# Kernel tuning notes

Measured on AMD Instinct MI355X. Metric: run time of the kernel, lower is better.

The kernel has to match this reference:

```python
import jax, jax.numpy as jnp
import numpy as np

N = 50000
IN_CH = 128
HID = 256
HEADS = 8
HEAD_DIM = HID // HEADS
NUM_CLASSES = 2
E = 800000
NEG_SLOPE = 0.2  # PyG GATConv default leaky_relu slope


def gat_conv(x, edge_index, W, att_src, att_dst, bias):
    """PyG-style GATConv (concat=True, add_self_loops=True, eval mode).
    x: [N, HID]; edge_index: [2, E] (row 0 = source j, row 1 = target i).
    W: [HID, HEADS*HEAD_DIM]; att_src/att_dst: [HEADS, HEAD_DIM]; bias: [HEADS*HEAD_DIM].
    """
    loop = jnp.arange(N)
    src = jnp.concatenate([edge_index[0], loop])  # self-loops appended
    dst = jnp.concatenate([edge_index[1], loop])
    h = (x @ W).reshape(N, HEADS, HEAD_DIM)          # [N, H, D]
    a_src = jnp.einsum('nhd,hd->nh', h, att_src)     # [N, H]
    a_dst = jnp.einsum('nhd,hd->nh', h, att_dst)
    e = jax.nn.leaky_relu(a_src[src] + a_dst[dst], NEG_SLOPE)  # [E+N, H]
    # segment softmax over incoming edges of each target node
    m = jax.ops.segment_max(e, dst, num_segments=N)
    p = jnp.exp(e - m[dst])
    s = jax.ops.segment_sum(p, dst, num_segments=N)
    alpha = p / (s[dst] + 1e-16)                     # [E+N, H]
    msg = h[src] * alpha[:, :, None]                 # [E+N, H, D]
    out = jax.ops.segment_sum(msg, dst, num_segments=N)  # [N, H, D]
    return out.reshape(N, HEADS * HEAD_DIM) + bias


def setup_inputs() -> dict:
    key = jax.random.key(0)
    ks = jax.random.split(key, 24)
    g = lambda k, shape, fan_in: jax.random.normal(k, shape, dtype=jnp.float32) / np.sqrt(fan_in)
    inp = {}
    inp['x'] = jax.random.normal(ks[0], (N, IN_CH), dtype=jnp.float32)
    inp['tut_edge_index'] = jax.random.randint(ks[1], (2, E), 0, N)
    inp['tdt_edge_index'] = jax.random.randint(ks[2], (2, E), 0, N)
    inp['proj_W'] = g(ks[3], (IN_CH, HID), IN_CH)
    inp['proj_b'] = jnp.zeros((HID,), jnp.float32)
    # 2 GAT layers per meta-path, stacked on leading axis
    inp['tut_W'] = g(ks[4], (2, HID, HID), HID)
    inp['tut_asrc'] = g(ks[5], (2, HEADS, HEAD_DIM), HEAD_DIM)
    inp['tut_adst'] = g(ks[6], (2, HEADS, HEAD_DIM), HEAD_DIM)
    inp['tut_bias'] = jnp.zeros((2, HID), jnp.float32)
    inp['tdt_W'] = g(ks[7], (2, HID, HID), HID)
    inp['tdt_asrc'] = g(ks[8], (2, HEADS, HEAD_DIM), HEAD_DIM)
    inp['tdt_adst'] = g(ks[9], (2, HEADS, HEAD_DIM), HEAD_DIM)
    inp['tdt_bias'] = jnp.zeros((2, HID), jnp.float32)
    inp['sem_att'] = jnp.full((2,), 0.5, jnp.float32)
    inp['cls_W1'] = g(ks[10], (HID, HID // 2), HID)
    inp['cls_b1'] = jnp.zeros((HID // 2,), jnp.float32)
    inp['cls_W2'] = g(ks[11], (HID // 2, NUM_CLASSES), HID // 2)
    inp['cls_b2'] = jnp.zeros((NUM_CLASSES,), jnp.float32)
    return inp


def reference(x, tut_edge_index, tdt_edge_index, proj_W, proj_b,
              tut_W, tut_asrc, tut_adst, tut_bias,
              tdt_W, tdt_asrc, tdt_adst, tdt_bias,
              sem_att, cls_W1, cls_b1, cls_W2, cls_b2):
    h = x @ proj_W + proj_b
    # TUT branch: 2 GATConv layers (eval mode -> dropout is identity)
    h_tut = h
    for l in range(2):
        h_tut = gat_conv(h_tut, tut_edge_index, tut_W[l], tut_asrc[l], tut_adst[l], tut_bias[l])
        h_tut = jax.nn.elu(h_tut)
    # TDT branch
    h_tdt = h
    for l in range(2):
        h_tdt = gat_conv(h_tdt, tdt_edge_index, tdt_W[l], tdt_asrc[l], tdt_adst[l], tdt_bias[l])
        h_tdt = jax.nn.elu(h_tdt)
    w = jax.nn.softmax(sem_att)
    z = w[0] * h_tut + w[1] * h_tdt
    hc = jax.nn.relu(z @ cls_W1 + cls_b1)
    logits = hc @ cls_W2 + cls_b2  # [N, NUM_CLASSES]
    return logits
```

## Files before the change

### kernel.cpp

```cpp
#include <hip/hip_runtime.h>
#include <hip/hip_fp16.h>
#include <cstddef>
#include <cstdint>


#define HID        256
#define HEADS      8
#define NEG_SLOPE  0.2f

#define BSH     7
#define BNODES  128
#define MAXNB   512
#define CH      2048

typedef __attribute__((ext_vector_type(8))) short short8v;
typedef __attribute__((ext_vector_type(4))) float float4v;

static __device__ __forceinline__ unsigned short f32_to_bf16(float v) {
    union { float f; unsigned u; } c; c.f = v;
    unsigned r = c.u + 0x7FFFu + ((c.u >> 16) & 1u);
    return (unsigned short)(r >> 16);
}
static __device__ __forceinline__ float bf16_to_f32(unsigned short b) {
    union { unsigned u; float f; } c; c.u = ((unsigned)b) << 16;
    return c.f;
}
static __device__ __forceinline__ void split_bf16(float v, unsigned short& hi, unsigned short& lo) {
    hi = f32_to_bf16(v);
    lo = f32_to_bf16(v - bf16_to_f32(hi));
}
static __device__ __forceinline__ void gload_lds16(const void* g, void* l) {
    __builtin_amdgcn_global_load_lds((const __attribute__((address_space(1))) void*)g,
                                     (__attribute__((address_space(3))) void*)l, 16, 0, 0);
}

template<int MODE>
__global__ __launch_bounds__(256) void mfma_gemm_kernel(
    const unsigned short* __restrict__ Ahi, const unsigned short* __restrict__ Alo,
    const unsigned short* __restrict__ Bthi, const unsigned short* __restrict__ Btlo,
    const float* __restrict__ bias,
    unsigned short* __restrict__ Chi, unsigned short* __restrict__ Clo,
    __half* __restrict__ Cf16a, __half* __restrict__ Cf16b, float* __restrict__ Cf32,
    int M, int N, int K)
{
    __shared__ __align__(16) short lds[4 * 4096];

    const int tid  = threadIdx.x;
    const int lane = tid & 63;
    const int w    = tid >> 6;
    const int wr   = w >> 1;
    const int wc   = w & 1;
    const int m0   = blockIdx.y * 128;
    const int n0   = blockIdx.x * 128;

    const unsigned short* sbase = (w == 0) ? Ahi : (w == 1) ? Alo : (w == 2) ? Bthi : Btlo;
    const int rowbase = (w < 2) ? m0 : n0;
    const int rowlim  = ((w < 2) ? M : N) - 1;

    float4v acc[4][4];
    #pragma unroll
    for (int i = 0; i < 4; ++i)
        #pragma unroll
        for (int j = 0; j < 4; ++j)
            acc[i][j] = (float4v){0.f, 0.f, 0.f, 0.f};

    const int kcl = lane >> 4;
    const int rl  = lane & 15;

    for (int k0 = 0; k0 < K; k0 += 32) {
        #pragma unroll
        for (int rh = 0; rh < 2; ++rh) {
            int row = rowbase + rh * 64 + lane;
            row = row > rowlim ? rowlim : row;
            const unsigned short* src = sbase + (size_t)row * K + k0;
            #pragma unroll
            for (int kc = 0; kc < 4; ++kc) {
                short* dst = &lds[w * 4096 + kc * 1024 + rh * 512];
                gload_lds16(src + kc * 8, dst);
            }
        }
        __syncthreads();

        short8v ahi[4], alo[4], bhi[4], blo[4];
        #pragma unroll
        for (int i = 0; i < 4; ++i) {
            int am = wr * 64 + i * 16 + rl;
            int bn = wc * 64 + i * 16 + rl;
            ahi[i] = *(const short8v*)&lds[0 * 4096 + kcl * 1024 + am * 8];
            alo[i] = *(const short8v*)&lds[1 * 4096 + kcl * 1024 + am * 8];
            bhi[i] = *(const short8v*)&lds[2 * 4096 + kcl * 1024 + bn * 8];
            blo[i] = *(const short8v*)&lds[3 * 4096 + kcl * 1024 + bn * 8];
        }
        #pragma unroll
        for (int i = 0; i < 4; ++i)
            #pragma unroll
            for (int j = 0; j < 4; ++j) {
                acc[i][j] = __builtin_amdgcn_mfma_f32_16x16x32_bf16(ahi[i], bhi[j], acc[i][j], 0, 0, 0);
                acc[i][j] = __builtin_amdgcn_mfma_f32_16x16x32_bf16(ahi[i], blo[j], acc[i][j], 0, 0, 0);
                acc[i][j] = __builtin_amdgcn_mfma_f32_16x16x32_bf16(alo[i], bhi[j], acc[i][j], 0, 0, 0);
            }
        __syncthreads();
    }

    const int cr = (lane >> 4) * 4;
    #pragma unroll
    for (int i = 0; i < 4; ++i) {
        #pragma unroll
        for (int r = 0; r < 4; ++r) {
            int row = m0 + wr * 64 + i * 16 + cr + r;
            if (row >= M) continue;
            #pragma unroll
            for (int j = 0; j < 4; ++j) {
                int col = n0 + wc * 64 + j * 16 + rl;
                float v = acc[i][j][r];
                if (bias) v += bias[col];
                if (MODE == 0) {
                    unsigned short h, l;
                    split_bf16(v, h, l);
                    Chi[(size_t)row * N + col] = h;
                    Clo[(size_t)row * N + col] = l;
                } else if (MODE == 1) {
                    if (col < 256) Cf16a[(size_t)row * 256 + col] = __float2half(v);
                    else           Cf16b[(size_t)row * 256 + (col - 256)] = __float2half(v);
                } else {
                    Cf32[(size_t)row * N + col] = fmaxf(v, 0.f);
                }
            }
        }
    }
}

__global__ void prep_kernel(
    const float* __restrict__ proj_W, const float* __restrict__ tut_W,
    const float* __restrict__ tdt_W, const float* __restrict__ cls_W1,
    unsigned short* __restrict__ pWthi, unsigned short* __restrict__ pWtlo,
    unsigned short* __restrict__ w1hi,  unsigned short* __restrict__ w1lo,
    unsigned short* __restrict__ t2Whi, unsigned short* __restrict__ t2Wlo,
    unsigned short* __restrict__ d2Whi, unsigned short* __restrict__ d2Wlo,
    unsigned short* __restrict__ cWthi, unsigned short* __restrict__ cWtlo,
    const float* __restrict__ x,
    unsigned short* __restrict__ xhi, unsigned short* __restrict__ xlo, int count4x)
{
    const int tid = blockIdx.x * blockDim.x + threadIdx.x;
    const int stride = gridDim.x * blockDim.x;
    for (int idx = tid; idx < 327680; idx += stride) {
        unsigned short h, l;
        if (idx < 32768) {
            int k = idx >> 8, n = idx & 255;
            split_bf16(proj_W[idx], h, l);
            pWthi[n * 128 + k] = h; pWtlo[n * 128 + k] = l;
        } else if (idx < 163840) {
            int r = idx - 32768;
            int ly = r >> 16, rr = r & 65535;
            int k = rr >> 8, n = rr & 255;
            split_bf16(tut_W[r], h, l);
            if (ly == 0) { w1hi[n * 256 + k] = h;  w1lo[n * 256 + k] = l; }
            else         { t2Whi[n * 256 + k] = h; t2Wlo[n * 256 + k] = l; }
        } else if (idx < 294912) {
            int r = idx - 163840;
            int ly = r >> 16, rr = r & 65535;
            int k = rr >> 8, n = rr & 255;
            split_bf16(tdt_W[r], h, l);
            if (ly == 0) { w1hi[(256 + n) * 256 + k] = h; w1lo[(256 + n) * 256 + k] = l; }
            else         { d2Whi[n * 256 + k] = h;        d2Wlo[n * 256 + k] = l; }
        } else {
            int r = idx - 294912;
            int k = r >> 7, n = r & 127;
            split_bf16(cls_W1[r], h, l);
            cWthi[n * 256 + k] = h; cWtlo[n * 256 + k] = l;
        }
    }
    for (int i = tid; i < count4x; i += stride) {
        float4 v = reinterpret_cast<const float4*>(x)[i];
        ushort4 hh, ll;
        split_bf16(v.x, hh.x, ll.x);
        split_bf16(v.y, hh.y, ll.y);
        split_bf16(v.z, hh.z, ll.z);
        split_bf16(v.w, hh.w, ll.w);
        reinterpret_cast<ushort4*>(xhi)[i] = hh;
        reinterpret_cast<ushort4*>(xlo)[i] = ll;
    }
}

__global__ __launch_bounds__(256) void att_kernel(
    const __half* __restrict__ hW,
    const float* __restrict__ att_src, const float* __restrict__ att_dst,
    float* __restrict__ a_src, float* __restrict__ a_dst, int n_nodes)
{
    const int wave = threadIdx.x >> 6;
    const int lane = threadIdx.x & 63;
    const int n = blockIdx.x * 4 + wave;
    if (n >= n_nodes) return;

    const __half2* hp = reinterpret_cast<const __half2*>(&hW[(size_t)n * HID + lane * 4]);
    __half2 h01 = hp[0], h23 = hp[1];
    float hx = __low2float(h01), hy = __high2float(h01);
    float hz = __low2float(h23), hw = __high2float(h23);
    float4 s4 = *reinterpret_cast<const float4*>(&att_src[lane * 4]);
    float4 d4 = *reinterpret_cast<const float4*>(&att_dst[lane * 4]);
    float ps = hx * s4.x + hy * s4.y + hz * s4.z + hw * s4.w;
    float pd = hx * d4.x + hy * d4.y + hz * d4.z + hw * d4.w;
    #pragma unroll
    for (int off = 1; off < 8; off <<= 1) {
        ps += __shfl_xor(ps, off);
        pd += __shfl_xor(pd, off);
    }
    if ((lane & 7) == 0) {
        a_src[n * HEADS + (lane >> 3)] = ps;
        a_dst[n * HEADS + (lane >> 3)] = pd;
    }
}

template<int OMODE>
__global__ __launch_bounds__(256) void gat_kernel(
    const __half* __restrict__ hW,
    const float* __restrict__ a_src, const float* __restrict__ a_dst,
    const int* __restrict__ row_ptr, const int* __restrict__ adj,
    const float* __restrict__ bias,
    const unsigned short* __restrict__ prevHi, const unsigned short* __restrict__ prevLo,
    const float* __restrict__ sem,
    unsigned short* __restrict__ outhi, unsigned short* __restrict__ outlo,
    int n_nodes)
{
    const int wave = threadIdx.x >> 6;
    const int lane = threadIdx.x & 63;
    const int n = blockIdx.x * 4 + wave;
    if (n >= n_nodes) return;

    const int beg = row_ptr[n];
    const int end = row_ptr[n + 1];
    const int h1 = lane & 7;
    const float adst1 = a_dst[n * HEADS + h1];

    float m = -INFINITY, s = 0.f;
    for (int j = beg + (lane >> 3); j < end; j += 8) {
        float e = a_src[adj[j] * HEADS + h1] + adst1;
        e = (e > 0.f) ? e : NEG_SLOPE * e;
        float mn = fmaxf(m, e);
        float t = (m > -INFINITY) ? s * __expf(m - mn) : 0.f;
        s = t + __expf(e - mn);
        m = mn;
    }
    #pragma unroll
    for (int off = 8; off < 64; off <<= 1) {
        float mo = __shfl_xor(m, off);
        float so = __shfl_xor(s, off);
        float mn = fmaxf(m, mo);
        float t1 = (m  > -INFINITY) ? s  * __expf(m  - mn) : 0.f;
        float t2 = (mo > -INFINITY) ? so * __expf(mo - mn) : 0.f;
        s = t1 + t2;
        m = mn;
    }

    const int h2 = lane >> 3;
    const float mh  = __shfl(m, h2);
    const float sh  = __shfl(s, h2);
    const float inv = 1.f / (sh + 1e-16f);
    const float adst2 = a_dst[n * HEADS + h2];
    const int lane4 = lane * 4;

    float4 acc = make_float4(0.f, 0.f, 0.f, 0.f);
    int j = beg;
    for (; j + 4 <= end; j += 4) {
        int s0 = adj[j + 0], s1 = adj[j + 1], s2 = adj[j + 2], s3 = adj[j + 3];
        float e0 = a_src[s0 * HEADS + h2] + adst2;
        float e1 = a_src[s1 * HEADS + h2] + adst2;
        float e2 = a_src[s2 * HEADS + h2] + adst2;
        float e3 = a_src[s3 * HEADS + h2] + adst2;
        e0 = (e0 > 0.f) ? e0 : NEG_SLOPE * e0;
        e1 = (e1 > 0.f) ? e1 : NEG_SLOPE * e1;
        e2 = (e2 > 0.f) ? e2 : NEG_SLOPE * e2;
        e3 = (e3 > 0.f) ? e3 : NEG_SLOPE * e3;
        float al0 = __expf(e0 - mh) * inv;
        float al1 = __expf(e1 - mh) * inv;
        float al2 = __expf(e2 - mh) * inv;
        float al3 = __expf(e3 - mh) * inv;
        const __half2* p0 = reinterpret_cast<const __half2*>(&hW[(size_t)s0 * HID + lane4]);
        const __half2* p1 = reinterpret_cast<const __half2*>(&hW[(size_t)s1 * HID + lane4]);
        const __half2* p2 = reinterpret_cast<const __half2*>(&hW[(size_t)s2 * HID + lane4]);
        const __half2* p3 = reinterpret_cast<const __half2*>(&hW[(size_t)s3 * HID + lane4]);
        __half2 a01 = p0[0], a23 = p0[1];
        __half2 b01 = p1[0], b23 = p1[1];
        __half2 c01 = p2[0], c23 = p2[1];
        __half2 d01 = p3[0], d23 = p3[1];
        acc.x += al0 * __low2float(a01); acc.y += al0 * __high2float(a01);
        acc.z += al0 * __low2float(a23); acc.w += al0 * __high2float(a23);
        acc.x += al1 * __low2float(b01); acc.y += al1 * __high2float(b01);
        acc.z += al1 * __low2float(b23); acc.w += al1 * __high2float(b23);
        acc.x += al2 * __low2float(c01); acc.y += al2 * __high2float(c01);
        acc.z += al2 * __low2float(c23); acc.w += al2 * __high2float(c23);
        acc.x += al3 * __low2float(d01); acc.y += al3 * __high2float(d01);
        acc.z += al3 * __low2float(d23); acc.w += al3 * __high2float(d23);
    }
    for (; j < end; ++j) {
        int src = adj[j];
        float e = a_src[src * HEADS + h2] + adst2;
        e = (e > 0.f) ? e : NEG_SLOPE * e;
        float alpha = __expf(e - mh) * inv;
        const __half2* p = reinterpret_cast<const __half2*>(&hW[(size_t)src * HID + lane4]);
        __half2 a01 = p[0], a23 = p[1];
        acc.x += alpha * __low2float(a01); acc.y += alpha * __high2float(a01);
        acc.z += alpha * __low2float(a23); acc.w += alpha * __high2float(a23);
    }

    float4 bv = *reinterpret_cast<const float4*>(&bias[lane4]);
    float4 o;
    o.x = acc.x + bv.x; o.y = acc.y + bv.y; o.z = acc.z + bv.z; o.w = acc.w + bv.w;
    o.x = (o.x > 0.f) ? o.x : expm1f(o.x);
    o.y = (o.y > 0.f) ? o.y : expm1f(o.y);
    o.z = (o.z > 0.f) ? o.z : expm1f(o.z);
    o.w = (o.w > 0.f) ? o.w : expm1f(o.w);

    if (OMODE == 1) {
        const float e0 = __expf(sem[0]);
        const float e1 = __expf(sem[1]);
        const float w0 = e0 / (e0 + e1);
        const float w1 = e1 / (e0 + e1);
        ushort4 ph = *reinterpret_cast<const ushort4*>(&prevHi[(size_t)n * HID + lane4]);
        ushort4 pl = *reinterpret_cast<const ushort4*>(&prevLo[(size_t)n * HID + lane4]);
        o.x = w0 * (bf16_to_f32(ph.x) + bf16_to_f32(pl.x)) + w1 * o.x;
        o.y = w0 * (bf16_to_f32(ph.y) + bf16_to_f32(pl.y)) + w1 * o.y;
        o.z = w0 * (bf16_to_f32(ph.z) + bf16_to_f32(pl.z)) + w1 * o.z;
        o.w = w0 * (bf16_to_f32(ph.w) + bf16_to_f32(pl.w)) + w1 * o.w;
    }

    ushort4 oh, ol;
    split_bf16(o.x, oh.x, ol.x);
    split_bf16(o.y, oh.y, ol.y);
    split_bf16(o.z, oh.z, ol.z);
    split_bf16(o.w, oh.w, ol.w);
    *reinterpret_cast<ushort4*>(&outhi[(size_t)n * HID + lane4]) = oh;
    *reinterpret_cast<ushort4*>(&outlo[(size_t)n * HID + lane4]) = ol;
}

__global__ __launch_bounds__(256) void bucket_count_kernel(
    const int* __restrict__ tut_dst, const int* __restrict__ tdt_dst,
    int* __restrict__ gcount, int E, int NB)
{
    __shared__ int hist[MAXNB];
    const int g = blockIdx.y;
    const int* dstp = g ? tdt_dst : tut_dst;
    for (int i = threadIdx.x; i < MAXNB; i += 256) hist[i] = 0;
    __syncthreads();
    for (int e = blockIdx.x * 256 + threadIdx.x; e < E; e += gridDim.x * 256)
        atomicAdd(&hist[dstp[e] >> BSH], 1);
    __syncthreads();
    for (int i = threadIdx.x; i < NB; i += 256) {
        int c = hist[i];
        if (c) atomicAdd(&gcount[g * NB + i], c);
    }
}

__global__ __launch_bounds__(512) void bucket_scan_kernel(
    const int* __restrict__ gcount, int* __restrict__ ebase, int* __restrict__ adjbase,
    int* __restrict__ rp0, int* __restrict__ rp1, int N, int E, int NB)
{
    __shared__ int sa[MAXNB], sb[MAXNB];
    const int t = threadIdx.x;
    for (int g = 0; g < 2; ++g) {
        int cnt = (t < NB) ? gcount[g * NB + t] : 0;
        int nodes = 0;
        if (t < NB) { int s = t << BSH; nodes = (N - s < BNODES) ? (N - s) : BNODES; }
        sa[t] = cnt;
        sb[t] = cnt + nodes;
        __syncthreads();
        for (int off = 1; off < MAXNB; off <<= 1) {
            int va = (t >= off) ? sa[t - off] : 0;
            int vb = (t >= off) ? sb[t - off] : 0;
            __syncthreads();
            sa[t] += va; sb[t] += vb;
            __syncthreads();
        }
        if (t < NB) {
            ebase[g * (NB + 1) + t + 1] = sa[t];
            adjbase[g * (NB + 1) + t + 1] = sb[t];
        }
        if (t == 0) { ebase[g * (NB + 1)] = 0; adjbase[g * (NB + 1)] = 0; }
        __syncthreads();
    }
    if (t == 0) { rp0[N] = E + N; rp1[N] = E + N; }
}

__global__ __launch_bounds__(256) void bucket_bin_kernel(
    const int* __restrict__ tut_ei, const int* __restrict__ tdt_ei,
    const int* __restrict__ ebase, int* __restrict__ gcursor,
    int* __restrict__ ebuf, int E, int NB)
{
    __shared__ int lhist[MAXNB];
    __shared__ int lbase[MAXNB];
    __shared__ int loffs[MAXNB];
    __shared__ int spair[CH];
    __shared__ int saddr[CH];
    const int g = blockIdx.y;
    const int* ei = g ? tdt_ei : tut_ei;
    const int e0 = blockIdx.x * CH;
    const int cnt = (E - e0 < CH) ? (E - e0) : CH;

    for (int i = threadIdx.x; i < MAXNB; i += 256) lhist[i] = 0;
    __syncthreads();

    int myb[8], myrank[8], mypk[8];
    int nmine = 0;
    #pragma unroll
    for (int k = 0; k < 8; ++k) {
        int idx = e0 + threadIdx.x + k * 256;
        if (idx < e0 + cnt) {
            int sv = ei[idx];
            int dv = ei[E + idx];
            int b = dv >> BSH;
            int r = atomicAdd(&lhist[b], 1);
            myb[nmine] = b; myrank[nmine] = r;
            mypk[nmine] = (sv << BSH) | (dv & (BNODES - 1));
            ++nmine;
        }
    }
    __syncthreads();
    loffs[threadIdx.x] = lhist[threadIdx.x];
    loffs[threadIdx.x + 256] = lhist[threadIdx.x + 256];
    __syncthreads();
    for (int off = 1; off < MAXNB; off <<= 1) {
        int i0 = threadIdx.x, i1 = threadIdx.x + 256;
        int v0 = (i0 >= off) ? loffs[i0 - off] : 0;
        int v1 = (i1 >= off) ? loffs[i1 - off] : 0;
        __syncthreads();
        loffs[i0] += v0; loffs[i1] += v1;
        __syncthreads();
    }
    for (int i = threadIdx.x; i < NB; i += 256) {
        int c = lhist[i];
        lbase[i] = c ? atomicAdd(&gcursor[g * NB + i], c) : 0;
    }
    __syncthreads();
    const int* eb = ebase + g * (NB + 1);
    for (int k = 0; k < nmine; ++k) {
        int b = myb[k];
        int sorted = loffs[b] - lhist[b] + myrank[k];
        spair[sorted] = mypk[k];
        saddr[sorted] = eb[b] + lbase[b] + myrank[k];
    }
    __syncthreads();
    int* out = ebuf + (size_t)g * E;
    for (int i = threadIdx.x; i < cnt; i += 256)
        out[saddr[i]] = spair[i];
}

__global__ __launch_bounds__(256) void bucket_csr_kernel(
    const int* __restrict__ gcount, const int* __restrict__ ebase,
    const int* __restrict__ adjbase, const int* __restrict__ ebuf,
    int* __restrict__ rp0, int* __restrict__ rp1,
    int* __restrict__ adj0, int* __restrict__ adj1, int N, int E, int NB)
{
    __shared__ int hist[BNODES], scn[BNODES], cursor[BNODES];
    const int g = blockIdx.y;
    const int b = blockIdx.x;
    int* rp  = g ? rp1 : rp0;
    int* adj = g ? adj1 : adj0;
    const int cnt = gcount[g * NB + b];
    const int aB  = adjbase[g * (NB + 1) + b];
    const int node0 = b << BSH;
    const int nb = (N - node0 < BNODES) ? (N - node0) : BNODES;
    const int* ep = ebuf + (size_t)g * E + ebase[g * (NB + 1) + b];
    const int t = threadIdx.x;

    if (t < BNODES) hist[t] = 0;
    __syncthreads();
    for (int e = t; e < cnt; e += 256)
        atomicAdd(&hist[ep[e] & (BNODES - 1)], 1);
    __syncthreads();
    if (t < BNODES) scn[t] = (t < nb) ? hist[t] + 1 : 0;
    __syncthreads();
    for (int off = 1; off < BNODES; off <<= 1) {
        int v = 0;
        if (t < BNODES && t >= off) v = scn[t - off];
        __syncthreads();
        if (t < BNODES) scn[t] += v;
        __syncthreads();
    }
    if (t < nb) {
        int s = scn[t] - hist[t] - 1;
        rp[node0 + t] = aB + s;
        adj[aB + s] = node0 + t;
        cursor[t] = s + 1;
    }
    __syncthreads();
    for (int e = t; e < cnt; e += 256) {
        int p = ep[e];
        int pos = atomicAdd(&cursor[p & (BNODES - 1)], 1);
        adj[aB + pos] = p >> BSH;
    }
}

__global__ __launch_bounds__(256) void cls2_kernel(
    const float* __restrict__ hc, const float* __restrict__ W2,
    const float* __restrict__ b2, float* __restrict__ out, int n_nodes)
{
    const int wave = threadIdx.x >> 6;
    const int lane = threadIdx.x & 63;
    const int n = blockIdx.x * 4 + wave;
    if (n >= n_nodes) return;
    float h0 = hc[(size_t)n * 128 + lane];
    float h1 = hc[(size_t)n * 128 + 64 + lane];
    float p0 = h0 * W2[lane * 2 + 0] + h1 * W2[(64 + lane) * 2 + 0];
    float p1 = h0 * W2[lane * 2 + 1] + h1 * W2[(64 + lane) * 2 + 1];
    #pragma unroll
    for (int off = 1; off < 64; off <<= 1) {
        p0 += __shfl_xor(p0, off);
        p1 += __shfl_xor(p1, off);
    }
    if (lane == 0) {
        out[(size_t)n * 2 + 0] = p0 + b2[0];
        out[(size_t)n * 2 + 1] = p1 + b2[1];
    }
}

extern "C" void kernel_launch(void* const* d_in, const int* in_sizes, int n_in,
                              void* d_out, int out_size, void* d_ws, size_t ws_size,
                              hipStream_t stream)
{
    const float* x        = (const float*)d_in[0];
    const int*   tut_ei   = (const int*)d_in[1];
    const int*   tdt_ei   = (const int*)d_in[2];
    const float* proj_W   = (const float*)d_in[3];
    const float* proj_b   = (const float*)d_in[4];
    const float* tut_W    = (const float*)d_in[5];
    const float* tut_asrc = (const float*)d_in[6];
    const float* tut_adst = (const float*)d_in[7];
    const float* tut_bias = (const float*)d_in[8];
    const float* tdt_W    = (const float*)d_in[9];
    const float* tdt_asrc = (const float*)d_in[10];
    const float* tdt_adst = (const float*)d_in[11];
    const float* tdt_bias = (const float*)d_in[12];
    const float* sem_att  = (const float*)d_in[13];
    const float* cls_W1   = (const float*)d_in[14];
    const float* cls_b1   = (const float*)d_in[15];
    const float* cls_W2   = (const float*)d_in[16];
    const float* cls_b2   = (const float*)d_in[17];

    const int IN_CH = 128;
    const int N = in_sizes[0] / IN_CH;
    const int E = in_sizes[1] / 2;
    const int NB = (N + BNODES - 1) >> BSH;
    const size_t NH = (size_t)N * HID;
    const size_t NI = (size_t)N * IN_CH;

    char* base = (char*)d_ws;
    size_t off = 0;
    auto alloc = [&](size_t bytes) -> void* {
        void* p = base + off;
        off = (off + bytes + 255) & ~(size_t)255;
        return p;
    };
    unsigned short* xhi   = (unsigned short*)alloc(NI * 2);
    unsigned short* xlo   = (unsigned short*)alloc(NI * 2);
    unsigned short* t2lo  = (unsigned short*)alloc(NH * 2);
    unsigned short* h0hi  = (unsigned short*)alloc(NH * 2);
    unsigned short* h0lo  = (unsigned short*)alloc(NH * 2);
    unsigned short* l1thi = (unsigned short*)alloc(NH * 2);
    unsigned short* l1tlo = (unsigned short*)alloc(NH * 2);
    __half*         hWa   = (__half*)alloc(NH * 2);
    float* as1 = (float*)alloc((size_t)N * HEADS * sizeof(float));
    float* ad1 = (float*)alloc((size_t)N * HEADS * sizeof(float));
    float* as2 = (float*)alloc((size_t)N * HEADS * sizeof(float));
    float* ad2 = (float*)alloc((size_t)N * HEADS * sizeof(float));
    unsigned short* pWthi = (unsigned short*)alloc(256 * 128 * 2);
    unsigned short* pWtlo = (unsigned short*)alloc(256 * 128 * 2);
    unsigned short* w1hi  = (unsigned short*)alloc(512 * 256 * 2);
    unsigned short* w1lo  = (unsigned short*)alloc(512 * 256 * 2);
    unsigned short* t2Whi = (unsigned short*)alloc(256 * 256 * 2);
    unsigned short* t2Wlo = (unsigned short*)alloc(256 * 256 * 2);
    unsigned short* d2Whi = (unsigned short*)alloc(256 * 256 * 2);
    unsigned short* d2Wlo = (unsigned short*)alloc(256 * 256 * 2);
    unsigned short* cWthi = (unsigned short*)alloc(128 * 256 * 2);
    unsigned short* cWtlo = (unsigned short*)alloc(128 * 256 * 2);
    int* rp_tut  = (int*)alloc((size_t)(N + 1) * sizeof(int));
    int* adj_tut = (int*)alloc((size_t)(E + N) * sizeof(int));
    int* rp_tdt  = (int*)alloc((size_t)(N + 1) * sizeof(int));
    int* adj_tdt = (int*)alloc((size_t)(E + N) * sizeof(int));
    int* gbuf    = (int*)alloc((size_t)4 * NB * sizeof(int));
    int* gcount  = gbuf;
    int* gcursor = gbuf + 2 * NB;
    int* ebase   = (int*)alloc((size_t)2 * (NB + 1) * sizeof(int));
    int* adjbase = (int*)alloc((size_t)2 * (NB + 1) * sizeof(int));
    (void)ws_size; (void)n_in; (void)out_size;

    int* ebuf = (int*)hWa;
    __half* hWb = (__half*)t2lo;
    unsigned short* t2hi = xhi;
    unsigned short* l1dhi = h0hi;
    unsigned short* l1dlo = h0lo;
    unsigned short* zhi = l1thi;
    unsigned short* zlo = l1tlo;
    float* hc = (float*)hWa;

    const int nodeBlocks = (N + 3) / 4;

    hipMemsetAsync(gbuf, 0, (size_t)4 * NB * sizeof(int), stream);
    prep_kernel<<<1024, 256, 0, stream>>>(proj_W, tut_W, tdt_W, cls_W1,
                                          pWthi, pWtlo, w1hi, w1lo, t2Whi, t2Wlo,
                                          d2Whi, d2Wlo, cWthi, cWtlo,
                                          x, xhi, xlo, (int)(NI / 4));
    bucket_count_kernel<<<dim3(128, 2), 256, 0, stream>>>(tut_ei + E, tdt_ei + E, gcount, E, NB);
    bucket_scan_kernel<<<1, 512, 0, stream>>>(gcount, ebase, adjbase, rp_tut, rp_tdt, N, E, NB);
    bucket_bin_kernel<<<dim3((E + CH - 1) / CH, 2), 256, 0, stream>>>(
        tut_ei, tdt_ei, ebase, gcursor, ebuf, E, NB);
    bucket_csr_kernel<<<dim3(NB, 2), 256, 0, stream>>>(
        gcount, ebase, adjbase, ebuf, rp_tut, rp_tdt, adj_tut, adj_tdt, N, E, NB);

    const int gy = (N + 127) / 128;
    const int AS = HEADS * (HID / HEADS);

    mfma_gemm_kernel<0><<<dim3(2, gy), 256, 0, stream>>>(
        xhi, xlo, pWthi, pWtlo, proj_b, h0hi, h0lo, nullptr, nullptr, nullptr,
        N, HID, IN_CH);

    mfma_gemm_kernel<1><<<dim3(4, gy), 256, 0, stream>>>(
        h0hi, h0lo, w1hi, w1lo, nullptr, nullptr, nullptr, hWa, hWb, nullptr,
        N, 512, HID);
    att_kernel<<<nodeBlocks, 256, 0, stream>>>(hWa, tut_asrc, tut_adst, as1, ad1, N);
    att_kernel<<<nodeBlocks, 256, 0, stream>>>(hWb, tdt_asrc, tdt_adst, as2, ad2, N);
    gat_kernel<0><<<nodeBlocks, 256, 0, stream>>>(
        hWa, as1, ad1, rp_tut, adj_tut, tut_bias,
        nullptr, nullptr, nullptr, l1thi, l1tlo, N);
    gat_kernel<0><<<nodeBlocks, 256, 0, stream>>>(
        hWb, as2, ad2, rp_tdt, adj_tdt, tdt_bias,
        nullptr, nullptr, nullptr, l1dhi, l1dlo, N);

    mfma_gemm_kernel<1><<<dim3(2, gy), 256, 0, stream>>>(
        l1thi, l1tlo, t2Whi, t2Wlo, nullptr, nullptr, nullptr, hWa, nullptr, nullptr,
        N, HID, HID);
    att_kernel<<<nodeBlocks, 256, 0, stream>>>(hWa, tut_asrc + AS, tut_adst + AS, as1, ad1, N);
    gat_kernel<0><<<nodeBlocks, 256, 0, stream>>>(
        hWa, as1, ad1, rp_tut, adj_tut, tut_bias + HID,
        nullptr, nullptr, nullptr, t2hi, t2lo, N);

    mfma_gemm_kernel<1><<<dim3(2, gy), 256, 0, stream>>>(
        l1dhi, l1dlo, d2Whi, d2Wlo, nullptr, nullptr, nullptr, hWa, nullptr, nullptr,
        N, HID, HID);
    att_kernel<<<nodeBlocks, 256, 0, stream>>>(hWa, tdt_asrc + AS, tdt_adst + AS, as2, ad2, N);
    gat_kernel<1><<<nodeBlocks, 256, 0, stream>>>(
        hWa, as2, ad2, rp_tdt, adj_tdt, tdt_bias + HID,
        t2hi, t2lo, sem_att, zhi, zlo, N);

    mfma_gemm_kernel<2><<<dim3(1, gy), 256, 0, stream>>>(
        zhi, zlo, cWthi, cWtlo, cls_b1, nullptr, nullptr, nullptr, nullptr, hc,
        N, 128, HID);
    cls2_kernel<<<nodeBlocks, 256, 0, stream>>>(hc, cls_W2, cls_b2, (float*)d_out, N);
}
```

Before: 728.7 us.

## Fuse attention logits into GEMM epilogue, double-buffer LDS, swizzle blocks across XCDs

Computes per-head attention source and destination scores inside the MODE 1 GEMM epilogue using the fp32 accumulators and cross-lane shuffles, which removes four att_kernel launches and their re-reads of the fp16 projected features. The GEMM K loop now double-buffers LDS, prefetching the next K slice while MFMAs run on the current one. Workgroup indices are remapped so neighbouring tiles land on the same XCD. The costs are twice the LDS per block, which may lower occupancy, and attention scores now computed from fp32 values instead of rounded fp16.

```diff
diff --git a/kernel.cpp b/kernel.cpp
--- a/kernel.cpp
+++ b/kernel.cpp
@@ -41,17 +41,29 @@
     const float* __restrict__ bias,
     unsigned short* __restrict__ Chi, unsigned short* __restrict__ Clo,
     __half* __restrict__ Cf16a, __half* __restrict__ Cf16b, float* __restrict__ Cf32,
+    const float* __restrict__ sW0, const float* __restrict__ dW0,
+    const float* __restrict__ sW1, const float* __restrict__ dW1,
+    float* __restrict__ oS0, float* __restrict__ oD0,
+    float* __restrict__ oS1, float* __restrict__ oD1,
     int M, int N, int K)
 {
-    __shared__ __align__(16) short lds[4 * 4096];
+    __shared__ __align__(16) short lds[2][4 * 4096];
 
     const int tid  = threadIdx.x;
     const int lane = tid & 63;
     const int w    = tid >> 6;
     const int wr   = w >> 1;
     const int wc   = w & 1;
-    const int m0   = blockIdx.y * 128;
-    const int n0   = blockIdx.x * 128;
+
+    const int gx   = gridDim.x;
+    const int nwg  = gx * gridDim.y;
+    const int flat = blockIdx.y * gx + blockIdx.x;
+    const int q    = nwg >> 3, r8 = nwg & 7;
+    const int xcd  = flat & 7, idx = flat >> 3;
+    const int swz  = (xcd < r8) ? xcd * (q + 1) + idx
+                                : r8 * (q + 1) + (xcd - r8) * q + idx;
+    const int m0   = (swz / gx) * 128;
+    const int n0   = (swz % gx) * 128;
 
     const unsigned short* sbase = (w == 0) ? Ahi : (w == 1) ? Alo : (w == 2) ? Bthi : Btlo;
     const int rowbase = (w < 2) ? m0 : n0;
@@ -67,7 +79,7 @@
     const int kcl = lane >> 4;
     const int rl  = lane & 15;
 
-    for (int k0 = 0; k0 < K; k0 += 32) {
+    auto stage = [&](int buf, int k0) {
         #pragma unroll
         for (int rh = 0; rh < 2; ++rh) {
             int row = rowbase + rh * 64 + lane;
@@ -75,21 +87,28 @@
             const unsigned short* src = sbase + (size_t)row * K + k0;
             #pragma unroll
             for (int kc = 0; kc < 4; ++kc) {
-                short* dst = &lds[w * 4096 + kc * 1024 + rh * 512];
+                short* dst = &lds[buf][w * 4096 + kc * 1024 + rh * 512];
                 gload_lds16(src + kc * 8, dst);
             }
         }
-        __syncthreads();
+    };
+
+    stage(0, 0);
+    __syncthreads();
+
+    int buf = 0;
+    for (int k0 = 0; k0 < K; k0 += 32) {
+        if (k0 + 32 < K) stage(buf ^ 1, k0 + 32);
 
         short8v ahi[4], alo[4], bhi[4], blo[4];
         #pragma unroll
         for (int i = 0; i < 4; ++i) {
             int am = wr * 64 + i * 16 + rl;
             int bn = wc * 64 + i * 16 + rl;
-            ahi[i] = *(const short8v*)&lds[0 * 4096 + kcl * 1024 + am * 8];
-            alo[i] = *(const short8v*)&lds[1 * 4096 + kcl * 1024 + am * 8];
-            bhi[i] = *(const short8v*)&lds[2 * 4096 + kcl * 1024 + bn * 8];
-            blo[i] = *(const short8v*)&lds[3 * 4096 + kcl * 1024 + bn * 8];
+            ahi[i] = *(const short8v*)&lds[buf][0 * 4096 + kcl * 1024 + am * 8];
+            alo[i] = *(const short8v*)&lds[buf][1 * 4096 + kcl * 1024 + am * 8];
+            bhi[i] = *(const short8v*)&lds[buf][2 * 4096 + kcl * 1024 + bn * 8];
+            blo[i] = *(const short8v*)&lds[buf][3 * 4096 + kcl * 1024 + bn * 8];
         }
         #pragma unroll
         for (int i = 0; i < 4; ++i)
@@ -100,15 +119,25 @@
                 acc[i][j] = __builtin_amdgcn_mfma_f32_16x16x32_bf16(alo[i], bhi[j], acc[i][j], 0, 0, 0);
             }
         __syncthreads();
-    }
-
-    const int cr = (lane >> 4) * 4;
+        buf ^= 1;
+    }
+
+    const int cr = kcl * 4;
+    const int cbase = n0 + wc * 64;
+    const int hA = ((cbase & 255) >> 5);
+    const bool g1 = (cbase >= 256);
+    const float* sW = g1 ? sW1 : sW0;
+    const float* dW = g1 ? dW1 : dW0;
+    float* oS = g1 ? oS1 : oS0;
+    float* oD = g1 ? oD1 : oD0;
+
     #pragma unroll
     for (int i = 0; i < 4; ++i) {
         #pragma unroll
         for (int r = 0; r < 4; ++r) {
             int row = m0 + wr * 64 + i * 16 + cr + r;
             if (row >= M) continue;
+            float ps0 = 0.f, pd0 = 0.f, ps1 = 0.f, pd1 = 0.f;
             #pragma unroll
             for (int j = 0; j < 4; ++j) {
                 int col = n0 + wc * 64 + j * 16 + rl;
@@ -122,8 +151,27 @@
                 } else if (MODE == 1) {
                     if (col < 256) Cf16a[(size_t)row * 256 + col] = __float2half(v);
                     else           Cf16b[(size_t)row * 256 + (col - 256)] = __float2half(v);
+                    int ac = col & 255;
+                    float sw = sW[ac], dw = dW[ac];
+                    if (j < 2) { ps0 += v * sw; pd0 += v * dw; }
+                    else       { ps1 += v * sw; pd1 += v * dw; }
                 } else {
                     Cf32[(size_t)row * N + col] = fmaxf(v, 0.f);
+                }
+            }
+            if (MODE == 1) {
+                #pragma unroll
+                for (int o = 1; o < 16; o <<= 1) {
+                    ps0 += __shfl_xor(ps0, o);
+                    pd0 += __shfl_xor(pd0, o);
+                    ps1 += __shfl_xor(ps1, o);
+                    pd1 += __shfl_xor(pd1, o);
+                }
+                if (rl == 0) {
+                    oS[(size_t)row * HEADS + hA]     = ps0;
+                    oS[(size_t)row * HEADS + hA + 1] = ps1;
+                    oD[(size_t)row * HEADS + hA]     = pd0;
+                    oD[(size_t)row * HEADS + hA + 1] = pd1;
                 }
             }
         }
@@ -179,35 +227,6 @@
         split_bf16(v.w, hh.w, ll.w);
         reinterpret_cast<ushort4*>(xhi)[i] = hh;
         reinterpret_cast<ushort4*>(xlo)[i] = ll;
-    }
-}
-
-__global__ __launch_bounds__(256) void att_kernel(
-    const __half* __restrict__ hW,
-    const float* __restrict__ att_src, const float* __restrict__ att_dst,
-    float* __restrict__ a_src, float* __restrict__ a_dst, int n_nodes)
-{
-    const int wave = threadIdx.x >> 6;
-    const int lane = threadIdx.x & 63;
-    const int n = blockIdx.x * 4 + wave;
-    if (n >= n_nodes) return;
-
-    const __half2* hp = reinterpret_cast<const __half2*>(&hW[(size_t)n * HID + lane * 4]);
-    __half2 h01 = hp[0], h23 = hp[1];
-    float hx = __low2float(h01), hy = __high2float(h01);
-    float hz = __low2float(h23), hw = __high2float(h23);
-    float4 s4 = *reinterpret_cast<const float4*>(&att_src[lane * 4]);
-    float4 d4 = *reinterpret_cast<const float4*>(&att_dst[lane * 4]);
-    float ps = hx * s4.x + hy * s4.y + hz * s4.z + hw * s4.w;
-    float pd = hx * d4.x + hy * d4.y + hz * d4.z + hw * d4.w;
-    #pragma unroll
-    for (int off = 1; off < 8; off <<= 1) {
-        ps += __shfl_xor(ps, off);
-        pd += __shfl_xor(pd, off);
-    }
-    if ((lane & 7) == 0) {
-        a_src[n * HEADS + (lane >> 3)] = ps;
-        a_dst[n * HEADS + (lane >> 3)] = pd;
     }
 }
 
@@ -611,13 +630,13 @@
 
     mfma_gemm_kernel<0><<<dim3(2, gy), 256, 0, stream>>>(
         xhi, xlo, pWthi, pWtlo, proj_b, h0hi, h0lo, nullptr, nullptr, nullptr,
+        nullptr, nullptr, nullptr, nullptr, nullptr, nullptr, nullptr, nullptr,
         N, HID, IN_CH);
 
     mfma_gemm_kernel<1><<<dim3(4, gy), 256, 0, stream>>>(
         h0hi, h0lo, w1hi, w1lo, nullptr, nullptr, nullptr, hWa, hWb, nullptr,
+        tut_asrc, tut_adst, tdt_asrc, tdt_adst, as1, ad1, as2, ad2,
         N, 512, HID);
-    att_kernel<<<nodeBlocks, 256, 0, stream>>>(hWa, tut_asrc, tut_adst, as1, ad1, N);
-    att_kernel<<<nodeBlocks, 256, 0, stream>>>(hWb, tdt_asrc, tdt_adst, as2, ad2, N);
     gat_kernel<0><<<nodeBlocks, 256, 0, stream>>>(
         hWa, as1, ad1, rp_tut, adj_tut, tut_bias,
         nullptr, nullptr, nullptr, l1thi, l1tlo, N);
@@ -627,22 +646,23 @@
 
     mfma_gemm_kernel<1><<<dim3(2, gy), 256, 0, stream>>>(
         l1thi, l1tlo, t2Whi, t2Wlo, nullptr, nullptr, nullptr, hWa, nullptr, nullptr,
+        tut_asrc + AS, tut_adst + AS, tut_asrc + AS, tut_adst + AS, as1, ad1, as1, ad1,
         N, HID, HID);
-    att_kernel<<<nodeBlocks, 256, 0, stream>>>(hWa, tut_asrc + AS, tut_adst + AS, as1, ad1, N);
     gat_kernel<0><<<nodeBlocks, 256, 0, stream>>>(
         hWa, as1, ad1, rp_tut, adj_tut, tut_bias + HID,
         nullptr, nullptr, nullptr, t2hi, t2lo, N);
 
     mfma_gemm_kernel<1><<<dim3(2, gy), 256, 0, stream>>>(
         l1dhi, l1dlo, d2Whi, d2Wlo, nullptr, nullptr, nullptr, hWa, nullptr, nullptr,
+        tdt_asrc + AS, tdt_adst + AS, tdt_asrc + AS, tdt_adst + AS, as2, ad2, as2, ad2,
         N, HID, HID);
-    att_kernel<<<nodeBlocks, 256, 0, stream>>>(hWa, tdt_asrc + AS, tdt_adst + AS, as2, ad2, N);
     gat_kernel<1><<<nodeBlocks, 256, 0, stream>>>(
         hWa, as2, ad2, rp_tdt, adj_tdt, tdt_bias + HID,
         t2hi, t2lo, sem_att, zhi, zlo, N);
 
     mfma_gemm_kernel<2><<<dim3(1, gy), 256, 0, stream>>>(
         zhi, zlo, cWthi, cWtlo, cls_b1, nullptr, nullptr, nullptr, nullptr, hc,
+        nullptr, nullptr, nullptr, nullptr, nullptr, nullptr, nullptr, nullptr,
         N, 128, HID);
     cls2_kernel<<<nodeBlocks, 256, 0, stream>>>(hc, cls_W2, cls_b2, (float*)d_out, N);
 }
```

Result: slower. 743.4 us (+2.0%).
